# Optimization experiments

Measured on AMD Instinct MI355X. Metric: run time of the kernel, lower is better.

The kernel has to match this reference:

```python
import jax, jax.numpy as jnp
import numpy as np

CHAN = 24
INNER = 64
GROUPS = 8
M = 5
LAM = 1e-4
MAX_ITER = 25
BETA = 1.0
EPS = 1e-5
B, HH, WW = 128, 32, 32


def conv2d(x, w, b=None):
    # NCHW, OIHW, 3x3 SAME conv (padding = kernel//2)
    y = jax.lax.conv_general_dilated(x, w, (1, 1), 'SAME',
                                     dimension_numbers=('NCHW', 'OIHW', 'NCHW'))
    if b is not None:
        y = y + b[None, :, None, None]
    return y


def group_norm(x, g, b):
    bsz, c, h, w = x.shape
    xg = x.reshape(bsz, GROUPS, c // GROUPS, h, w)
    mu = xg.mean(axis=(2, 3, 4), keepdims=True)
    var = xg.var(axis=(2, 3, 4), keepdims=True)
    xn = ((xg - mu) / jnp.sqrt(var + EPS)).reshape(bsz, c, h, w)
    return xn * g[None, :, None, None] + b[None, :, None, None]


def batch_norm(x, g, b):
    # training-mode batch statistics over (N, H, W)
    mu = x.mean(axis=(0, 2, 3), keepdims=True)
    var = x.var(axis=(0, 2, 3), keepdims=True)
    return (x - mu) / jnp.sqrt(var + EPS) * g[None, :, None, None] + b[None, :, None, None]


def resnet_f(p, z, x):
    c1w, g1g, g1b, c2w, g2g, g2b, g3g, g3b = p
    y = group_norm(jax.nn.relu(conv2d(z, c1w)), g1g, g1b)
    return group_norm(jax.nn.relu(z + group_norm(x + conv2d(y, c2w), g2g, g2b)), g3g, g3b)


def anderson(f, x0):
    # Anderson acceleration, fixed MAX_ITER iterations (no host-sync tol break).
    bsz = x0.shape[0]
    d = x0.size // bsz
    X = jnp.zeros((bsz, M, d), x0.dtype)
    Fm = jnp.zeros((bsz, M, d), x0.dtype)
    f0 = f(x0).reshape(bsz, -1)
    X = X.at[:, 0].set(x0.reshape(bsz, -1))
    Fm = Fm.at[:, 0].set(f0)
    X = X.at[:, 1].set(f0)
    Fm = Fm.at[:, 1].set(f(f0.reshape(x0.shape)).reshape(bsz, -1))
    for k in range(2, MAX_ITER):
        n = min(k, M)
        G = Fm[:, :n] - X[:, :n]                       # [b, n, d]
        Hm = jnp.zeros((bsz, n + 1, n + 1), x0.dtype)
        Hm = Hm.at[:, 0, 1:].set(1.0).at[:, 1:, 0].set(1.0)
        Hm = Hm.at[:, 1:, 1:].set(jnp.einsum('bnd,bmd->bnm', G, G)
                                  + LAM * jnp.eye(n, dtype=x0.dtype)[None])
        yv = jnp.zeros((bsz, n + 1, 1), x0.dtype).at[:, 0, 0].set(1.0)
        alpha = jnp.linalg.solve(Hm, yv)[:, 1:, 0]     # [b, n]
        xnew = (BETA * jnp.einsum('bn,bnd->bd', alpha, Fm[:, :n])
                + (1.0 - BETA) * jnp.einsum('bn,bnd->bd', alpha, X[:, :n]))
        X = X.at[:, k % M].set(xnew)
        Fm = Fm.at[:, k % M].set(f(xnew.reshape(x0.shape)).reshape(bsz, -1))
    return X[:, (MAX_ITER - 1) % M].reshape(x0.shape)


def setup_inputs() -> dict:
    key = jax.random.key(0)
    ks = jax.random.split(key, 8)
    inp = {
        'x': jax.random.normal(ks[0], (B, 3, HH, WW), jnp.float32),
        'pre_conv_w': jax.random.normal(ks[1], (CHAN, 3, 3, 3), jnp.float32) * 0.1,
        'pre_conv_b': jnp.zeros((CHAN,), jnp.float32),
        'pre_bn_g': jnp.ones((CHAN,), jnp.float32),
        'pre_bn_b': jnp.zeros((CHAN,), jnp.float32),
        'f_conv1_w': jax.random.normal(ks[2], (INNER, CHAN, 3, 3), jnp.float32) * 0.01,
        'gn1_g': jnp.ones((INNER,), jnp.float32),
        'gn1_b': jnp.zeros((INNER,), jnp.float32),
        'f_conv2_w': jax.random.normal(ks[3], (CHAN, INNER, 3, 3), jnp.float32) * 0.01,
        'gn2_g': jnp.ones((CHAN,), jnp.float32),
        'gn2_b': jnp.zeros((CHAN,), jnp.float32),
        'gn3_g': jnp.ones((CHAN,), jnp.float32),
        'gn3_b': jnp.zeros((CHAN,), jnp.float32),
        'post_bn_g': jnp.ones((CHAN,), jnp.float32),
        'post_bn_b': jnp.zeros((CHAN,), jnp.float32),
        'fc_w': jax.random.normal(ks[4], (10, CHAN * 4 * 4), jnp.float32) * 0.05,
        'fc_b': jnp.zeros((10,), jnp.float32),
    }
    return inp


def reference(x, pre_conv_w, pre_conv_b, pre_bn_g, pre_bn_b,
              f_conv1_w, gn1_g, gn1_b, f_conv2_w, gn2_g, gn2_b, gn3_g, gn3_b,
              post_bn_g, post_bn_b, fc_w, fc_b):
    # pre: conv + BatchNorm
    xp = batch_norm(conv2d(x, pre_conv_w, pre_conv_b), pre_bn_g, pre_bn_b)
    p = (f_conv1_w, gn1_g, gn1_b, f_conv2_w, gn2_g, gn2_b, gn3_g, gn3_b)
    # DEQ fixed-point solve (eval path: train=False returns the fixed point)
    z_star = anderson(lambda z: resnet_f(p, z, xp), jnp.zeros_like(xp))
    z = resnet_f(p, z_star, xp)
    # post: relu -> BN -> avgpool(8,8) -> flatten -> linear
    h = batch_norm(jax.nn.relu(z), post_bn_g, post_bn_b)
    bsz, c, hh, ww = h.shape
    pooled = h.reshape(bsz, c, hh // 8, 8, ww // 8, 8).mean(axis=(3, 5))  # [B,C,4,4]
    return pooled.reshape(bsz, -1) @ fc_w.T + fc_b
```

## Files before the change

kernel.cpp:

```cpp
#include <hip/hip_runtime.h>
#include <hip/hip_bf16.h>

typedef __hip_bfloat16 bf16;
typedef unsigned short ushortT;
typedef __attribute__((ext_vector_type(8))) short short8;
typedef __attribute__((ext_vector_type(4))) float f32x4;

#define BB 128
#define CHAN 24
#define INNER 64
#define HW 1024
#define DD (CHAN*HW)

constexpr size_t cBD = (size_t)BB*DD;
constexpr size_t cYB = (size_t)BB*INNER*HW;

__device__ __attribute__((aligned(16))) ushortT g_xp[cBD];
__device__ __attribute__((aligned(16))) ushortT g_X[5*cBD];
__device__ __attribute__((aligned(16))) ushortT g_F[5*cBD];
__device__ __attribute__((aligned(16))) ushortT g_G[5*cBD];
__device__ __attribute__((aligned(16))) ushortT g_yb[cYB];
__device__ __attribute__((aligned(16))) ushortT g_tb[cBD];
__device__ __attribute__((aligned(16))) ushortT g_w1m[9*64*32];
__device__ __attribute__((aligned(16))) ushortT g_w2m[9*24*64];
__device__ __attribute__((aligned(16))) float g_stats2a[48];
__device__ __attribute__((aligned(16))) float g_stats2b[48];
__device__ __attribute__((aligned(16))) float g_gn1sum[BB*8*2];
__device__ __attribute__((aligned(16))) float g_gn2sum[BB*24*2];
__device__ __attribute__((aligned(16))) float g_gn3p[BB*4*16];
__device__ __attribute__((aligned(16))) float g_gramp[BB*4*5*5];
__device__ __attribute__((aligned(16))) float g_gram[BB*25];
__device__ __attribute__((aligned(16))) float g_pooled[BB*CHAN*16];
__device__ __attribute__((aligned(16))) float g_params[5120];
__device__ unsigned g_isbf16;

#define P_PCW 0
#define P_PCB 648
#define P_PBG 672
#define P_PBB 696
#define P_G1G 720
#define P_G1B 784
#define P_G2G 848
#define P_G2B 872
#define P_G3G 896
#define P_G3B 920
#define P_POG 944
#define P_POB 968
#define P_FCW 992
#define P_FCB 4832

__device__ __forceinline__ size_t aidx(int b, int icv, int pix){
  return (((size_t)b*3 + icv)*1024 + (size_t)pix)*8;
}
__device__ __forceinline__ float rdin(const void* p, int i){
  if (g_isbf16) return __bfloat162float(((const bf16*)p)[i]);
  return ((const float*)p)[i];
}
__device__ __forceinline__ float b2f(ushortT u){
  unsigned v = ((unsigned)u) << 16;
  return __builtin_bit_cast(float, v);
}
__device__ __forceinline__ ushortT f2b(float f){
  unsigned u = __builtin_bit_cast(unsigned, f);
  u += 0x7FFFu + ((u >> 16) & 1u);
  return (ushortT)(u >> 16);
}
__device__ __forceinline__ void ld24c(const ushortT* base, int b, int pix, float* o){
  #pragma unroll
  for (int icv=0;icv<3;icv++){
    short8 v = *(const short8*)&base[aidx(b,icv,pix)];
    #pragma unroll
    for (int j=0;j<8;j++) o[icv*8+j] = b2f((ushortT)v[j]);
  }
}
__device__ __forceinline__ void st24c(ushortT* base, int b, int pix, const float* i){
  #pragma unroll
  for (int icv=0;icv<3;icv++){
    short8 v;
    #pragma unroll
    for (int j=0;j<8;j++) v[j] = (short)f2b(i[icv*8+j]);
    *(short8*)&base[aidx(b,icv,pix)] = v;
  }
}

__global__ void detect_k(const void* g1g){
  if (threadIdx.x==0 && blockIdx.x==0){
    unsigned u = *(const unsigned*)g1g;
    g_isbf16 = (u == 0x3F803F80u) ? 1u : 0u;
  }
}

__global__ void cvt_params_k(const void* pcw, const void* pcb, const void* pbg, const void* pbb,
                             const void* g1g, const void* g1b, const void* g2g, const void* g2b,
                             const void* g3g, const void* g3b, const void* pog, const void* pob,
                             const void* fcw, const void* fcb){
  int t = threadIdx.x;
  for (int i=t;i<648;i+=256)  g_params[P_PCW+i]=rdin(pcw,i);
  for (int i=t;i<24;i+=256) { g_params[P_PCB+i]=rdin(pcb,i);
                              g_params[P_PBG+i]=rdin(pbg,i);
                              g_params[P_PBB+i]=rdin(pbb,i);
                              g_params[P_G2G+i]=rdin(g2g,i);
                              g_params[P_G2B+i]=rdin(g2b,i);
                              g_params[P_G3G+i]=rdin(g3g,i);
                              g_params[P_G3B+i]=rdin(g3b,i);
                              g_params[P_POG+i]=rdin(pog,i);
                              g_params[P_POB+i]=rdin(pob,i); }
  for (int i=t;i<64;i+=256) { g_params[P_G1G+i]=rdin(g1g,i);
                              g_params[P_G1B+i]=rdin(g1b,i); }
  for (int i=t;i<3840;i+=256) g_params[P_FCW+i]=rdin(fcw,i);
  for (int i=t;i<10;i+=256)   g_params[P_FCB+i]=rdin(fcb,i);
  for (int i=t;i<48;i+=256) { g_stats2a[i]=0.f; g_stats2b[i]=0.f; }
}

__global__ void wtm_k(const void* w1, const void* w2){
  int t = blockIdx.x*256 + threadIdx.x;
  if (t < 9*64*32){
    int ic = t & 31, oc = (t>>5)&63, s9 = t>>11;
    float v = (ic<24) ? rdin(w1, (oc*24+ic)*9 + s9) : 0.f;
    g_w1m[t] = f2b(v);
  }
  int u = t - 9*64*32;
  if (u >= 0 && u < 9*24*64){
    int ic = u & 63; int rest = u >> 6; int oc = rest % 24; int s9 = rest / 24;
    g_w2m[u] = f2b(rdin(w2, (oc*64+ic)*9 + s9));
  }
}

__global__ void zeroX0_k(){
  size_t i = ((size_t)blockIdx.x*256 + threadIdx.x)*8;
  short8 z = {0,0,0,0,0,0,0,0};
  *(short8*)&g_X[i] = z;
  if (blockIdx.x < 8) g_gn1sum[blockIdx.x*256 + threadIdx.x] = 0.f;
}
__global__ void copyF0toX1_k(){
  size_t i = ((size_t)blockIdx.x*256 + threadIdx.x)*8;
  *(short8*)&g_X[cBD + i] = *(const short8*)&g_F[i];
  if (blockIdx.x < 8) g_gn1sum[blockIdx.x*256 + threadIdx.x] = 0.f;
}

__global__ void preconv_k(const void* __restrict__ x){
  int id = blockIdx.x*256 + threadIdx.x;
  int b = id >> 10, pix = id & 1023;
  int yy = pix >> 5, xx = pix & 31;
  float acc[24];
  #pragma unroll
  for (int oc=0;oc<24;oc++) acc[oc] = g_params[P_PCB+oc];
  for (int ic=0; ic<3; ic++)
    for (int ky=0; ky<3; ky++){
      int gy = yy+ky-1; if (gy<0||gy>=32) continue;
      for (int kx=0;kx<3;kx++){
        int gx = xx+kx-1; if (gx<0||gx>=32) continue;
        float v = rdin(x, ((b*3+ic)*32+gy)*32+gx);
        #pragma unroll
        for (int oc=0;oc<24;oc++)
          acc[oc] += v * g_params[P_PCW+(oc*3+ic)*9+ky*3+kx];
      }
    }
  st24c(g_tb, b, pix, acc);
}

template<bool RELU>
__global__ void bnstat2_k(int which){
  const ushortT* src = (which==0) ? g_tb : (g_F + 4*cBD);
  float* dst = (which==0) ? g_stats2a : g_stats2b;
  __shared__ float sRed[48];
  int b = blockIdx.x >> 2, seg = blockIdx.x & 3;
  int t = threadIdx.x;
  if (t < 48) sRed[t] = 0.f;
  __syncthreads();
  int icv = t >> 6, pl = t & 63;
  float p0[8], p1[8];
  #pragma unroll
  for (int e=0;e<8;e++){ p0[e]=0.f; p1[e]=0.f; }
  for (int it=0; it<4; it++){
    int pix = seg*256 + it*64 + pl;
    short8 v = *(const short8*)&src[aidx(b,icv,pix)];
    #pragma unroll
    for (int e=0;e<8;e++){
      float f = b2f((ushortT)v[e]); if (RELU) f = fmaxf(f,0.f);
      p0[e]+=f; p1[e]+=f*f;
    }
  }
  #pragma unroll
  for (int e=0;e<8;e++){
    atomicAdd(&sRed[(icv*8+e)*2],   p0[e]);
    atomicAdd(&sRed[(icv*8+e)*2+1], p1[e]);
  }
  __syncthreads();
  if (t < 48) atomicAdd(&dst[t], sRed[t]);
}

__global__ void bn_apply_k(){
  int id = blockIdx.x*256+threadIdx.x;
  int b = id >> 10, pix = id & 1023;
  const float inv = 1.f/(BB*HW);
  float tv[24], ov[24];
  ld24c(g_tb, b, pix, tv);
  #pragma unroll
  for (int c=0;c<24;c++){
    float mean = g_stats2a[c*2]*inv;
    float var = fmaxf(g_stats2a[c*2+1]*inv - mean*mean, 0.f);
    float rstd = rsqrtf(var + 1e-5f);
    ov[c] = (tv[c]-mean)*rstd*g_params[P_PBG+c] + g_params[P_PBB+c];
  }
  st24c(g_xp, b, pix, ov);
}

__launch_bounds__(256, 2)
__global__ void conv1_k(int s){
  __shared__ ushortT sMem[29312];
  ushortT* sA = sMem;
  ushortT* sW = sMem + 10880;
  const int tid = threadIdx.x;
  const int lane = tid & 63, wv = tid >> 6;
  const int mLane = lane & 15, q = lane >> 4;
  const int b = blockIdx.x >> 2, yt = blockIdx.x & 3;
  const ushortT* __restrict__ Xs = g_X + (size_t)s*cBD;
  if (blockIdx.x < 24) g_gn2sum[blockIdx.x*256 + tid] = 0.f;
  for (int i = tid; i < 1360; i += 256){
    int icv = i & 3, apix = i >> 2;
    int yl = apix / 34, xl = apix - yl*34;
    int gy = yt*8 - 1 + yl, gx = xl - 1;
    short8 v = {0,0,0,0,0,0,0,0};
    if (gy >= 0 && gy < 32 && gx >= 0 && gx < 32 && icv < 3)
      v = *(const short8*)&Xs[aidx(b, icv, gy*32 + gx)];
    *(short8*)&sA[(size_t)(apix*4 + (icv ^ (apix&3)))*8] = v;
  }
  for (int i = tid; i < 2304; i += 256){
    int icv = i & 3, rest = i >> 2;
    int oc = rest & 63, s9 = rest >> 6;
    short8 v = *(const short8*)&g_w1m[(size_t)((s9*64 + oc)*32) + icv*8];
    *(short8*)&sW[(size_t)((s9*64+oc)*4 + (icv ^ (oc&3)))*8] = v;
  }
  __syncthreads();
  f32x4 acc[4][4];
  #pragma unroll
  for (int mt=0;mt<4;mt++)
    #pragma unroll
    for (int nt=0;nt<4;nt++) acc[mt][nt] = (f32x4){0.f,0.f,0.f,0.f};
  for (int s9=0; s9<9; s9++){
    int ky = s9/3, kx = s9 - ky*3;
    short8 bfr[4];
    #pragma unroll
    for (int nt=0;nt<4;nt++){
      int oc = nt*16 + mLane;
      bfr[nt] = *(const short8*)&sW[(size_t)((s9*64+oc)*4 + (q ^ (oc&3)))*8];
    }
    #pragma unroll
    for (int mt=0;mt<4;mt++){
      int g = wv*4+mt;
      int apix = ((g>>1) + ky)*34 + (g&1)*16 + mLane + kx;
      short8 afr = *(const short8*)&sA[(size_t)(apix*4 + (q ^ (apix&3)))*8];
      #pragma unroll
      for (int nt=0;nt<4;nt++)
        acc[mt][nt] = __builtin_amdgcn_mfma_f32_16x16x32_bf16(afr, bfr[nt], acc[mt][nt], 0,0,0);
    }
  }
  __syncthreads();
  ushortT* sOut = sMem;
  #pragma unroll
  for (int mt=0;mt<4;mt++){
    int g = wv*4+mt;
    #pragma unroll
    for (int nt=0;nt<4;nt++){
      int oc = nt*16 + mLane;
      #pragma unroll
      for (int r=0;r<4;r++){
        int pix = (g>>1)*32 + (g&1)*16 + q*4 + r;
        sOut[pix*64 + oc] = f2b(fmaxf(acc[mt][nt][r], 0.f));
      }
    }
  }
  __syncthreads();
  float s0=0.f, s1=0.f;
  size_t gbase = ((size_t)b*1024 + yt*256)*64;
  for (int c = tid; c < 2048; c += 256){
    short8 v = *(const short8*)&sOut[c*8];
    *(short8*)&g_yb[gbase + (size_t)c*8] = v;
    #pragma unroll
    for (int j=0;j<8;j++){ float f = b2f((ushortT)v[j]); s0 += f; s1 += f*f; }
  }
  s0 += __shfl_down(s0,32); s1 += __shfl_down(s1,32);
  s0 += __shfl_down(s0,16); s1 += __shfl_down(s1,16);
  s0 += __shfl_down(s0, 8); s1 += __shfl_down(s1, 8);
  if (lane < 8){
    atomicAdd(&g_gn1sum[(b*8+lane)*2],   s0);
    atomicAdd(&g_gn1sum[(b*8+lane)*2+1], s1);
  }
}

__launch_bounds__(256, 2)
__global__ void conv2_k(){
  __shared__ ushortT sMem[35584];
  __shared__ float sAff[128];
  ushortT* sA = sMem;
  ushortT* sW = sMem + 21760;
  const int tid = threadIdx.x;
  const int lane = tid & 63, wv = tid >> 6;
  const int mLane = lane & 15, q = lane >> 4;
  const int b = blockIdx.x >> 2, yt = blockIdx.x & 3;
  if (tid < 64){
    int c = tid, gr = c>>3;
    float S = g_gn1sum[(b*8+gr)*2], Q = g_gn1sum[(b*8+gr)*2+1];
    float mean = S*(1.f/8192.f);
    float var = fmaxf(Q*(1.f/8192.f) - mean*mean, 0.f);
    float rstd = rsqrtf(var + 1e-5f);
    float sc = rstd*g_params[P_G1G+c];
    sAff[c] = sc; sAff[64+c] = g_params[P_G1B+c] - mean*sc;
  }
  __syncthreads();
  for (int i = tid; i < 2720; i += 256){
    int icv = i & 7, apix = i >> 3;
    int yl = apix / 34, xl = apix - yl*34;
    int gy = yt*8 - 1 + yl, gx = xl - 1;
    short8 v = {0,0,0,0,0,0,0,0};
    if (gy >= 0 && gy < 32 && gx >= 0 && gx < 32){
      short8 raw = *(const short8*)&g_yb[((size_t)b*1024 + gy*32+gx)*64 + icv*8];
      #pragma unroll
      for (int j=0;j<8;j++){
        int c = icv*8+j;
        v[j] = (short)f2b(b2f((ushortT)raw[j])*sAff[c] + sAff[64+c]);
      }
    }
    *(short8*)&sA[(size_t)(apix*8 + (icv ^ (apix&7)))*8] = v;
  }
  for (int i = tid; i < 1728; i += 256){
    int icv = i & 7, rest = i >> 3;
    int oc = rest % 24, s9 = rest / 24;
    short8 v = *(const short8*)&g_w2m[(size_t)((s9*24+oc)*64) + icv*8];
    *(short8*)&sW[(size_t)((s9*24+oc)*8 + (icv ^ (oc&7)))*8] = v;
  }
  __syncthreads();
  f32x4 acc[4][2];
  #pragma unroll
  for (int mt=0;mt<4;mt++){ acc[mt][0]=(f32x4){0.f,0.f,0.f,0.f}; acc[mt][1]=(f32x4){0.f,0.f,0.f,0.f}; }
  const bool nt1ok = (mLane < 8);
  for (int s9=0; s9<9; s9++){
    int ky = s9/3, kx = s9 - ky*3;
    #pragma unroll
    for (int ks=0; ks<2; ks++){
      int ib = ks*4;
      short8 bfr[2];
      { int oc = mLane;
        bfr[0] = *(const short8*)&sW[(size_t)((s9*24+oc)*8 + ((ib+q) ^ (oc&7)))*8]; }
      if (nt1ok){
        int oc = 16 + mLane;
        bfr[1] = *(const short8*)&sW[(size_t)((s9*24+oc)*8 + ((ib+q) ^ (oc&7)))*8];
      } else bfr[1] = (short8){0,0,0,0,0,0,0,0};
      #pragma unroll
      for (int mt=0;mt<4;mt++){
        int g = wv*4+mt;
        int apix = ((g>>1) + ky)*34 + (g&1)*16 + mLane + kx;
        short8 afr = *(const short8*)&sA[(size_t)(apix*8 + ((ib+q) ^ (apix&7)))*8];
        acc[mt][0] = __builtin_amdgcn_mfma_f32_16x16x32_bf16(afr, bfr[0], acc[mt][0], 0,0,0);
        acc[mt][1] = __builtin_amdgcn_mfma_f32_16x16x32_bf16(afr, bfr[1], acc[mt][1], 0,0,0);
      }
    }
  }
  #pragma unroll
  for (int nt=0;nt<2;nt++){
    int oc = nt*16 + mLane;
    bool ok = (oc < 24);
    int icv = oc >> 3, e = oc & 7;
    float s0=0.f, s1=0.f;
    if (ok){
      #pragma unroll
      for (int mt=0;mt<4;mt++){
        int g = wv*4+mt;
        #pragma unroll
        for (int r=0;r<4;r++){
          int pix = (yt*8 + (g>>1))*32 + (g&1)*16 + q*4 + r;
          size_t o = aidx(b, icv, pix) + e;
          float v = acc[mt][nt][r] + b2f(g_xp[o]);
          g_tb[o] = f2b(v);
          s0 += v; s1 += v*v;
        }
      }
    }
    s0 += __shfl_down(s0,32); s1 += __shfl_down(s1,32);
    s0 += __shfl_down(s0,16); s1 += __shfl_down(s1,16);
    if (lane < 16 && ok){
      atomicAdd(&g_gn2sum[(b*24+oc)*2],   s0);
      atomicAdd(&g_gn2sum[(b*24+oc)*2+1], s1);
    }
  }
}

__launch_bounds__(256)
__global__ void fuse_a_k(int s){
  __shared__ float sM2[8], sR2[8], sSc2[24], sSb2[24];
  __shared__ float sRed[64];
  const int b = blockIdx.x>>2, seg = blockIdx.x&3;
  const int t = threadIdx.x;
  if (t < 8){
    float S = g_gn2sum[(b*24+t*3)*2]   + g_gn2sum[(b*24+t*3+1)*2]   + g_gn2sum[(b*24+t*3+2)*2];
    float Q = g_gn2sum[(b*24+t*3)*2+1] + g_gn2sum[(b*24+t*3+1)*2+1] + g_gn2sum[(b*24+t*3+2)*2+1];
    float m = S*(1.f/3072.f);
    sM2[t] = m;
    sR2[t] = rsqrtf(fmaxf(Q*(1.f/3072.f) - m*m, 0.f) + 1e-5f);
  }
  __syncthreads();
  if (t < 24){
    int g = t/3;
    float sc = sR2[g]*g_params[P_G2G+t];
    sSc2[t] = sc; sSb2[t] = g_params[P_G2B+t] - sM2[g]*sc;
  }
  __syncthreads();
  const int pix = seg*256 + t;
  float tv[24], xv[24];
  ld24c(g_tb, b, pix, tv);
  ld24c(g_X + (size_t)s*cBD, b, pix, xv);
  float p0[8], p1[8];
  #pragma unroll
  for (int g=0;g<8;g++){ p0[g]=0.f; p1[g]=0.f; }
  #pragma unroll
  for (int c=0;c<24;c++){
    int g = c/3;
    float v = fmaxf(xv[c] + tv[c]*sSc2[c] + sSb2[c], 0.f);
    p0[g] += v; p1[g] += v*v;
  }
  #pragma unroll
  for (int g=0;g<8;g++){
    for (int off=32;off>0;off>>=1){ p0[g]+=__shfl_down(p0[g],off,64); p1[g]+=__shfl_down(p1[g],off,64); }
  }
  int lane = t&63, wv = t>>6;
  if (lane==0){
    #pragma unroll
    for (int g=0;g<8;g++){ sRed[wv*16+g*2]=p0[g]; sRed[wv*16+g*2+1]=p1[g]; }
  }
  __syncthreads();
  if (t < 16){
    g_gn3p[(b*4+seg)*16 + t] = sRed[t]+sRed[16+t]+sRed[32+t]+sRed[48+t];
  }
}

__launch_bounds__(256)
__global__ void fuse_b_k(int s, int nv){
  __shared__ float sM2[8], sR2[8], sM3[8], sR3[8];
  __shared__ float sSc2[24], sSb2[24], sSc3[24], sSb3[24];
  __shared__ float sRedG[4][5];
  const int b = blockIdx.x>>2, seg = blockIdx.x&3;
  const int t = threadIdx.x;
  if (t < 8){
    float S = g_gn2sum[(b*24+t*3)*2]   + g_gn2sum[(b*24+t*3+1)*2]   + g_gn2sum[(b*24+t*3+2)*2];
    float Q = g_gn2sum[(b*24+t*3)*2+1] + g_gn2sum[(b*24+t*3+1)*2+1] + g_gn2sum[(b*24+t*3+2)*2+1];
    float m = S*(1.f/3072.f);
    sM2[t] = m;
    sR2[t] = rsqrtf(fmaxf(Q*(1.f/3072.f) - m*m, 0.f) + 1e-5f);
    float S3 = g_gn3p[(b*4+0)*16+t*2]   + g_gn3p[(b*4+1)*16+t*2]
             + g_gn3p[(b*4+2)*16+t*2]   + g_gn3p[(b*4+3)*16+t*2];
    float Q3 = g_gn3p[(b*4+0)*16+t*2+1] + g_gn3p[(b*4+1)*16+t*2+1]
             + g_gn3p[(b*4+2)*16+t*2+1] + g_gn3p[(b*4+3)*16+t*2+1];
    float m3 = S3*(1.f/3072.f);
    sM3[t] = m3;
    sR3[t] = rsqrtf(fmaxf(Q3*(1.f/3072.f) - m3*m3, 0.f) + 1e-5f);
  }
  __syncthreads();
  if (t < 24){
    int g = t/3;
    float sc2 = sR2[g]*g_params[P_G2G+t];
    sSc2[t] = sc2; sSb2[t] = g_params[P_G2B+t] - sM2[g]*sc2;
    float sc3 = sR3[g]*g_params[P_G3G+t];
    sSc3[t] = sc3; sSb3[t] = g_params[P_G3B+t] - sM3[g]*sc3;
  }
  __syncthreads();
  const int pix = seg*256 + t;
  float tv[24], xv[24], fv[24], gl[24];
  ld24c(g_tb, b, pix, tv);
  ld24c(g_X + (size_t)s*cBD, b, pix, xv);
  #pragma unroll
  for (int c=0;c<24;c++){
    float v = fmaxf(xv[c] + tv[c]*sSc2[c] + sSb2[c], 0.f);
    fv[c] = v*sSc3[c] + sSb3[c];
    float g = fv[c] - xv[c];
    gl[c] = b2f(f2b(g));
  }
  st24c(g_F + (size_t)s*cBD, b, pix, fv);
  st24c(g_G + (size_t)s*cBD, b, pix, gl);
  if (nv == 0) return;
  float part[5];
  #pragma unroll
  for (int j=0;j<5;j++) part[j]=0.f;
  #pragma unroll
  for (int j=0;j<5;j++){
    if (j>=nv) continue;
    float acc=0.f;
    if (j==s){
      #pragma unroll
      for (int c=0;c<24;c++) acc += gl[c]*gl[c];
    } else {
      float gv[24];
      ld24c(g_G + (size_t)j*cBD, b, pix, gv);
      #pragma unroll
      for (int c=0;c<24;c++) acc += gl[c]*gv[c];
    }
    part[j]=acc;
  }
  int lane = t&63, wv = t>>6;
  #pragma unroll
  for (int j=0;j<5;j++){
    float v = part[j];
    for (int off=32;off>0;off>>=1) v += __shfl_down(v,off,64);
    if (lane==0 && j<nv) sRedG[wv][j] = v;
  }
  __syncthreads();
  if (t < 5 && t < nv){
    float v = sRedG[0][t]+sRedG[1][t]+sRedG[2][t]+sRedG[3][t];
    g_gramp[((b*4+seg)*5 + s)*5 + t] = v;
  }
}

template<int N>
__device__ __forceinline__ void chol_alpha(const float Kf[5][5], float* alpha){
  double K[N][N];
  #pragma unroll
  for (int i=0;i<N;i++)
    #pragma unroll
    for (int j=0;j<N;j++)
      K[i][j] = (double)Kf[i][j] + (i==j ? 1e-4 : 0.0);
  #pragma unroll
  for (int c=0;c<N;c++){
    double d = K[c][c];
    #pragma unroll
    for (int k2=0;k2<c;k2++) d -= K[c][k2]*K[c][k2];
    d = sqrt(fmax(d, 1e-300));
    K[c][c] = d;
    double inv = 1.0/d;
    #pragma unroll
    for (int r=c+1;r<N;r++){
      double v = K[r][c];
      #pragma unroll
      for (int k2=0;k2<c;k2++) v -= K[r][k2]*K[c][k2];
      K[r][c] = v*inv;
    }
  }
  double y[N];
  #pragma unroll
  for (int i=0;i<N;i++){
    double v = 1.0;
    #pragma unroll
    for (int j=0;j<i;j++) v -= K[i][j]*y[j];
    y[i] = v / K[i][i];
  }
  double w[N];
  #pragma unroll
  for (int i=N-1;i>=0;i--){
    double v = y[i];
    #pragma unroll
    for (int j=i+1;j<N;j++) v -= K[j][i]*w[j];
    w[i] = v / K[i][i];
  }
  double sum = 0.0;
  #pragma unroll
  for (int i=0;i<N;i++) sum += w[i];
  double invs = 1.0/sum;
  #pragma unroll
  for (int i=0;i<N;i++) alpha[i] = (float)(w[i]*invs);
}

__global__ void xns_k(int s, int n, int rA, int nvA, int rB, int nvB){
  __shared__ float sAlpha[5];
  if (blockIdx.x < 8) g_gn1sum[blockIdx.x*256 + threadIdx.x] = 0.f;
  const int b = blockIdx.x >> 2, ch = blockIdx.x & 3;
  const int t = threadIdx.x;
  if (t == 0){
    float Kf[5][5];
    for (int i=0;i<n;i++)
      for (int j=0;j<n;j++) Kf[i][j] = g_gram[b*25 + i*5 + j];
    for (int j=0;j<nvA;j++){
      float v = g_gramp[((b*4+0)*5 + rA)*5 + j] + g_gramp[((b*4+1)*5 + rA)*5 + j]
              + g_gramp[((b*4+2)*5 + rA)*5 + j] + g_gramp[((b*4+3)*5 + rA)*5 + j];
      Kf[rA][j] = v; Kf[j][rA] = v;
    }
    if (rB >= 0){
      for (int j=0;j<nvB;j++){
        float v = g_gramp[((b*4+0)*5 + rB)*5 + j] + g_gramp[((b*4+1)*5 + rB)*5 + j]
                + g_gramp[((b*4+2)*5 + rB)*5 + j] + g_gramp[((b*4+3)*5 + rB)*5 + j];
        Kf[rB][j] = v; Kf[j][rB] = v;
      }
    }
    if (ch == 0){
      for (int j=0;j<nvA;j++){ g_gram[b*25+rA*5+j]=Kf[rA][j]; g_gram[b*25+j*5+rA]=Kf[rA][j]; }
      if (rB >= 0)
        for (int j=0;j<nvB;j++){ g_gram[b*25+rB*5+j]=Kf[rB][j]; g_gram[b*25+j*5+rB]=Kf[rB][j]; }
    }
    float al[5];
    if (n==2) chol_alpha<2>(Kf, al);
    else if (n==3) chol_alpha<3>(Kf, al);
    else if (n==4) chol_alpha<4>(Kf, al);
    else chol_alpha<5>(Kf, al);
    for (int j=0;j<n;j++) sAlpha[j] = al[j];
  }
  __syncthreads();
  float a[5];
  for (int j=0;j<n;j++) a[j] = sAlpha[j];
  const size_t base = (size_t)b*DD + (size_t)ch*6144;
  #pragma unroll
  for (int i=0;i<3;i++){
    size_t off = base + (size_t)i*2048 + (size_t)t*8;
    float acc[8];
    #pragma unroll
    for (int e=0;e<8;e++) acc[e]=0.f;
    for (int j=0;j<n;j++){
      short8 f = *(const short8*)&g_F[(size_t)j*cBD + off];
      float aj = a[j];
      #pragma unroll
      for (int e=0;e<8;e++) acc[e] += aj*b2f((ushortT)f[e]);
    }
    short8 o;
    #pragma unroll
    for (int e=0;e<8;e++) o[e] = (short)f2b(acc[e]);
    *(short8*)&g_X[(size_t)s*cBD + off] = o;
  }
}

__global__ void post_pool_k(){
  int i = blockIdx.x*256+threadIdx.x; if (i >= BB*CHAN*16) return;
  const ushortT* z = g_F + 4*cBD;
  int pw = i&3, ph=(i>>2)&3, c=(i>>4)%CHAN, bi=i/(CHAN*16);
  int icv = c>>3, e = c&7;
  float inv = 1.f/(BB*HW);
  float mean = g_stats2b[c*2]*inv;
  float var = fmaxf(g_stats2b[c*2+1]*inv - mean*mean, 0.f);
  float rstd = rsqrtf(var + 1e-5f);
  float gg=g_params[P_POG+c], bv=g_params[P_POB+c];
  float s=0.f;
  for (int dy=0;dy<8;dy++)
    for (int dx=0;dx<8;dx++){
      int pix = (ph*8+dy)*32 + pw*8+dx;
      float v = fmaxf(b2f(z[aidx(bi,icv,pix) + e]), 0.f);
      s += (v-mean)*rstd*gg + bv;
    }
  g_pooled[i] = s*(1.f/64.f);
}

__global__ void fc_k(void* __restrict__ out){
  int i = blockIdx.x*256+threadIdx.x; if (i>=BB*10) return;
  int j=i%10, bi=i/10;
  float s = g_params[P_FCB+j];
  for (int k=0;k<384;k++) s += g_pooled[bi*384+k]*g_params[P_FCW+j*384+k];
  if (g_isbf16) ((bf16*)out)[i] = __float2bfloat16(s);
  else ((float*)out)[i] = s;
}

extern "C" void kernel_launch(void* const* d_in, const int* in_sizes, int n_in,
                              void* d_out, int out_size, void* d_ws, size_t ws_size,
                              hipStream_t stream){
  const void* x   = d_in[0];
  const void* pcw = d_in[1];
  const void* pcb = d_in[2];
  const void* pbg = d_in[3];
  const void* pbb = d_in[4];
  const void* w1  = d_in[5];
  const void* g1g = d_in[6];
  const void* g1b = d_in[7];
  const void* w2  = d_in[8];
  const void* g2g = d_in[9];
  const void* g2b = d_in[10];
  const void* g3g = d_in[11];
  const void* g3b = d_in[12];
  const void* pog = d_in[13];
  const void* pob = d_in[14];
  const void* fcw = d_in[15];
  const void* fcb = d_in[16];
  (void)d_ws; (void)ws_size;

  const int gPix = (int)(BB*HW/256);

  auto feval = [&](int s, int nv){
    conv1_k<<<512,256,0,stream>>>(s);
    conv2_k<<<512,256,0,stream>>>();
    fuse_a_k<<<512,256,0,stream>>>(s);
    fuse_b_k<<<512,256,0,stream>>>(s, nv);
  };

  detect_k<<<1,64,0,stream>>>(g1g);
  cvt_params_k<<<1,256,0,stream>>>(pcw,pcb,pbg,pbb,g1g,g1b,g2g,g2b,g3g,g3b,pog,pob,fcw,fcb);
  wtm_k<<<126,256,0,stream>>>(w1, w2);

  preconv_k<<<gPix,256,0,stream>>>(x);
  bnstat2_k<false><<<512,192,0,stream>>>(0);
  bn_apply_k<<<gPix,256,0,stream>>>();

  zeroX0_k<<<1536,256,0,stream>>>();
  feval(0, 1);
  copyF0toX1_k<<<1536,256,0,stream>>>();
  feval(1, 2);

  for (int k=2;k<25;k++){
    int n = k<5 ? k : 5;
    int s = k%5;
    int nv = (k+1<5)?(k+1):5;
    if (k==2) xns_k<<<512,256,0,stream>>>(s, 2, 0, 1, 1, 2);
    else      xns_k<<<512,256,0,stream>>>(s, n, (k-1)%5, n, -1, 0);
    feval(s, (k<24) ? nv : 0);
  }

  bnstat2_k<true><<<512,192,0,stream>>>(1);
  post_pool_k<<<(BB*CHAN*16+255)/256,256,0,stream>>>();
  fc_k<<<(BB*10+255)/256,256,0,stream>>>(d_out);
}
```

Measured before the change: 1.577 ms.

## Fuse GroupNorm, Gram, Anderson solve and mixing into one per-sample kernel

Merges fuse_a, fuse_b and xns into a single 1024-thread-per-sample kernel. It computes GN2/GN3 stats in-block, writes F and G, builds the Gram row, solves for alpha in one thread and forms the next X directly. It also folds the BN stats into preconv, skips conv1 on the zero first iterate via zeroed yb, and merges the post-pool and FC kernels. Launches and global round-trips drop, at the cost of only 128 blocks for the fused step and a serial Cholesky inside the block.

```diff
diff --git a/kernel.cpp b/kernel.cpp
--- a/kernel.cpp
+++ b/kernel.cpp
@@ -27,10 +27,7 @@
 __device__ __attribute__((aligned(16))) float g_stats2b[48];
 __device__ __attribute__((aligned(16))) float g_gn1sum[BB*8*2];
 __device__ __attribute__((aligned(16))) float g_gn2sum[BB*24*2];
-__device__ __attribute__((aligned(16))) float g_gn3p[BB*4*16];
-__device__ __attribute__((aligned(16))) float g_gramp[BB*4*5*5];
 __device__ __attribute__((aligned(16))) float g_gram[BB*25];
-__device__ __attribute__((aligned(16))) float g_pooled[BB*CHAN*16];
 __device__ __attribute__((aligned(16))) float g_params[5120];
 __device__ unsigned g_isbf16;
 
@@ -126,19 +123,18 @@
   }
 }
 
-__global__ void zeroX0_k(){
-  size_t i = ((size_t)blockIdx.x*256 + threadIdx.x)*8;
+__global__ void zero0_k(){
+  size_t base = ((size_t)blockIdx.x*256 + threadIdx.x)*8;
   short8 z = {0,0,0,0,0,0,0,0};
-  *(short8*)&g_X[i] = z;
-  if (blockIdx.x < 8) g_gn1sum[blockIdx.x*256 + threadIdx.x] = 0.f;
-}
-__global__ void copyF0toX1_k(){
-  size_t i = ((size_t)blockIdx.x*256 + threadIdx.x)*8;
-  *(short8*)&g_X[cBD + i] = *(const short8*)&g_F[i];
-  if (blockIdx.x < 8) g_gn1sum[blockIdx.x*256 + threadIdx.x] = 0.f;
+  *(short8*)&g_yb[base] = z;
+  if (blockIdx.x < 1536) *(short8*)&g_X[base] = z;
+  int t = blockIdx.x*256 + threadIdx.x;
+  if (blockIdx.x < 8)  g_gn1sum[t] = 0.f;
+  if (blockIdx.x < 24) g_gn2sum[t] = 0.f;
 }
 
 __global__ void preconv_k(const void* __restrict__ x){
+  __shared__ float sR2d[4*48];
   int id = blockIdx.x*256 + threadIdx.x;
   int b = id >> 10, pix = id & 1023;
   int yy = pix >> 5, xx = pix & 31;
@@ -157,37 +153,18 @@
       }
     }
   st24c(g_tb, b, pix, acc);
-}
-
-template<bool RELU>
-__global__ void bnstat2_k(int which){
-  const ushortT* src = (which==0) ? g_tb : (g_F + 4*cBD);
-  float* dst = (which==0) ? g_stats2a : g_stats2b;
-  __shared__ float sRed[48];
-  int b = blockIdx.x >> 2, seg = blockIdx.x & 3;
-  int t = threadIdx.x;
-  if (t < 48) sRed[t] = 0.f;
-  __syncthreads();
-  int icv = t >> 6, pl = t & 63;
-  float p0[8], p1[8];
-  #pragma unroll
-  for (int e=0;e<8;e++){ p0[e]=0.f; p1[e]=0.f; }
-  for (int it=0; it<4; it++){
-    int pix = seg*256 + it*64 + pl;
-    short8 v = *(const short8*)&src[aidx(b,icv,pix)];
-    #pragma unroll
-    for (int e=0;e<8;e++){
-      float f = b2f((ushortT)v[e]); if (RELU) f = fmaxf(f,0.f);
-      p0[e]+=f; p1[e]+=f*f;
-    }
-  }
-  #pragma unroll
-  for (int e=0;e<8;e++){
-    atomicAdd(&sRed[(icv*8+e)*2],   p0[e]);
-    atomicAdd(&sRed[(icv*8+e)*2+1], p1[e]);
-  }
-  __syncthreads();
-  if (t < 48) atomicAdd(&dst[t], sRed[t]);
+  int lane = threadIdx.x & 63, wv = threadIdx.x >> 6;
+  #pragma unroll
+  for (int c=0;c<24;c++){
+    float r = acc[c], q = acc[c]*acc[c];
+    #pragma unroll
+    for (int off=32;off;off>>=1){ r += __shfl_down(r,off,64); q += __shfl_down(q,off,64); }
+    if (lane==0){ sR2d[wv*48+c*2]=r; sR2d[wv*48+c*2+1]=q; }
+  }
+  __syncthreads();
+  if (threadIdx.x < 48)
+    atomicAdd(&g_stats2a[threadIdx.x],
+      sR2d[threadIdx.x] + sR2d[48+threadIdx.x] + sR2d[96+threadIdx.x] + sR2d[144+threadIdx.x]);
 }
 
 __global__ void bn_apply_k(){
@@ -386,12 +363,66 @@
   }
 }
 
-__launch_bounds__(256)
-__global__ void fuse_a_k(int s){
-  __shared__ float sM2[8], sR2[8], sSc2[24], sSb2[24];
-  __shared__ float sRed[64];
-  const int b = blockIdx.x>>2, seg = blockIdx.x&3;
+template<int N>
+__device__ __forceinline__ void chol_alpha(const float Kf[5][5], float* alpha){
+  double K[N][N];
+  #pragma unroll
+  for (int i=0;i<N;i++)
+    #pragma unroll
+    for (int j=0;j<N;j++)
+      K[i][j] = (double)Kf[i][j] + (i==j ? 1e-4 : 0.0);
+  #pragma unroll
+  for (int c=0;c<N;c++){
+    double d = K[c][c];
+    #pragma unroll
+    for (int k2=0;k2<c;k2++) d -= K[c][k2]*K[c][k2];
+    d = sqrt(fmax(d, 1e-300));
+    K[c][c] = d;
+    double inv = 1.0/d;
+    #pragma unroll
+    for (int r=c+1;r<N;r++){
+      double v = K[r][c];
+      #pragma unroll
+      for (int k2=0;k2<c;k2++) v -= K[r][k2]*K[c][k2];
+      K[r][c] = v*inv;
+    }
+  }
+  double y[N];
+  #pragma unroll
+  for (int i=0;i<N;i++){
+    double v = 1.0;
+    #pragma unroll
+    for (int j=0;j<i;j++) v -= K[i][j]*y[j];
+    y[i] = v / K[i][i];
+  }
+  double w[N];
+  #pragma unroll
+  for (int i=N-1;i>=0;i--){
+    double v = y[i];
+    #pragma unroll
+    for (int j=i+1;j<N;j++) v -= K[j][i]*w[j];
+    w[i] = v / K[i][i];
+  }
+  double sum = 0.0;
+  #pragma unroll
+  for (int i=0;i<N;i++) sum += w[i];
+  double invs = 1.0/sum;
+  #pragma unroll
+  for (int i=0;i<N;i++) alpha[i] = (float)(w[i]*invs);
+}
+
+__launch_bounds__(1024)
+__global__ void fuse_k(int s, int n, int snext){
+  __shared__ float sM2[8], sR2[8], sM3[8], sR3[8];
+  __shared__ float sSc2[24], sSb2[24], sSc3[24], sSb3[24];
+  __shared__ float sRed[16*16];
+  __shared__ float sRedG[16*5];
+  __shared__ float sAlpha[5];
+  __shared__ float sStat[16*48];
+  const int b = blockIdx.x;
   const int t = threadIdx.x;
+  const int lane = t & 63, wv = t >> 6;
+  if (t < 16) g_gn1sum[b*16 + t] = 0.f;
   if (t < 8){
     float S = g_gn2sum[(b*24+t*3)*2]   + g_gn2sum[(b*24+t*3+1)*2]   + g_gn2sum[(b*24+t*3+2)*2];
     float Q = g_gn2sum[(b*24+t*3)*2+1] + g_gn2sum[(b*24+t*3+1)*2+1] + g_gn2sum[(b*24+t*3+2)*2+1];
@@ -406,241 +437,169 @@
     sSc2[t] = sc; sSb2[t] = g_params[P_G2B+t] - sM2[g]*sc;
   }
   __syncthreads();
-  const int pix = seg*256 + t;
-  float tv[24], xv[24];
-  ld24c(g_tb, b, pix, tv);
-  ld24c(g_X + (size_t)s*cBD, b, pix, xv);
+  float xv[24], v[24];
+  ld24c(g_tb, b, t, v);
+  ld24c(g_X + (size_t)s*cBD, b, t, xv);
   float p0[8], p1[8];
   #pragma unroll
   for (int g=0;g<8;g++){ p0[g]=0.f; p1[g]=0.f; }
   #pragma unroll
   for (int c=0;c<24;c++){
+    float val = fmaxf(xv[c] + v[c]*sSc2[c] + sSb2[c], 0.f);
+    v[c] = val;
     int g = c/3;
-    float v = fmaxf(xv[c] + tv[c]*sSc2[c] + sSb2[c], 0.f);
-    p0[g] += v; p1[g] += v*v;
+    p0[g] += val; p1[g] += val*val;
   }
   #pragma unroll
   for (int g=0;g<8;g++){
-    for (int off=32;off>0;off>>=1){ p0[g]+=__shfl_down(p0[g],off,64); p1[g]+=__shfl_down(p1[g],off,64); }
-  }
-  int lane = t&63, wv = t>>6;
+    #pragma unroll
+    for (int off=32;off;off>>=1){ p0[g]+=__shfl_down(p0[g],off,64); p1[g]+=__shfl_down(p1[g],off,64); }
+  }
   if (lane==0){
     #pragma unroll
     for (int g=0;g<8;g++){ sRed[wv*16+g*2]=p0[g]; sRed[wv*16+g*2+1]=p1[g]; }
   }
   __syncthreads();
-  if (t < 16){
-    g_gn3p[(b*4+seg)*16 + t] = sRed[t]+sRed[16+t]+sRed[32+t]+sRed[48+t];
-  }
-}
-
-__launch_bounds__(256)
-__global__ void fuse_b_k(int s, int nv){
-  __shared__ float sM2[8], sR2[8], sM3[8], sR3[8];
-  __shared__ float sSc2[24], sSb2[24], sSc3[24], sSb3[24];
-  __shared__ float sRedG[4][5];
-  const int b = blockIdx.x>>2, seg = blockIdx.x&3;
-  const int t = threadIdx.x;
   if (t < 8){
-    float S = g_gn2sum[(b*24+t*3)*2]   + g_gn2sum[(b*24+t*3+1)*2]   + g_gn2sum[(b*24+t*3+2)*2];
-    float Q = g_gn2sum[(b*24+t*3)*2+1] + g_gn2sum[(b*24+t*3+1)*2+1] + g_gn2sum[(b*24+t*3+2)*2+1];
+    float S=0.f, Q=0.f;
+    #pragma unroll
+    for (int w=0;w<16;w++){ S += sRed[w*16+t*2]; Q += sRed[w*16+t*2+1]; }
     float m = S*(1.f/3072.f);
-    sM2[t] = m;
-    sR2[t] = rsqrtf(fmaxf(Q*(1.f/3072.f) - m*m, 0.f) + 1e-5f);
-    float S3 = g_gn3p[(b*4+0)*16+t*2]   + g_gn3p[(b*4+1)*16+t*2]
-             + g_gn3p[(b*4+2)*16+t*2]   + g_gn3p[(b*4+3)*16+t*2];
-    float Q3 = g_gn3p[(b*4+0)*16+t*2+1] + g_gn3p[(b*4+1)*16+t*2+1]
-             + g_gn3p[(b*4+2)*16+t*2+1] + g_gn3p[(b*4+3)*16+t*2+1];
-    float m3 = S3*(1.f/3072.f);
-    sM3[t] = m3;
-    sR3[t] = rsqrtf(fmaxf(Q3*(1.f/3072.f) - m3*m3, 0.f) + 1e-5f);
+    sM3[t] = m;
+    sR3[t] = rsqrtf(fmaxf(Q*(1.f/3072.f) - m*m, 0.f) + 1e-5f);
   }
   __syncthreads();
   if (t < 24){
     int g = t/3;
-    float sc2 = sR2[g]*g_params[P_G2G+t];
-    sSc2[t] = sc2; sSb2[t] = g_params[P_G2B+t] - sM2[g]*sc2;
-    float sc3 = sR3[g]*g_params[P_G3G+t];
-    sSc3[t] = sc3; sSb3[t] = g_params[P_G3B+t] - sM3[g]*sc3;
-  }
-  __syncthreads();
-  const int pix = seg*256 + t;
-  float tv[24], xv[24], fv[24], gl[24];
-  ld24c(g_tb, b, pix, tv);
-  ld24c(g_X + (size_t)s*cBD, b, pix, xv);
-  #pragma unroll
-  for (int c=0;c<24;c++){
-    float v = fmaxf(xv[c] + tv[c]*sSc2[c] + sSb2[c], 0.f);
-    fv[c] = v*sSc3[c] + sSb3[c];
-    float g = fv[c] - xv[c];
-    gl[c] = b2f(f2b(g));
-  }
-  st24c(g_F + (size_t)s*cBD, b, pix, fv);
-  st24c(g_G + (size_t)s*cBD, b, pix, gl);
-  if (nv == 0) return;
-  float part[5];
-  #pragma unroll
-  for (int j=0;j<5;j++) part[j]=0.f;
-  #pragma unroll
-  for (int j=0;j<5;j++){
-    if (j>=nv) continue;
-    float acc=0.f;
-    if (j==s){
-      #pragma unroll
-      for (int c=0;c<24;c++) acc += gl[c]*gl[c];
-    } else {
-      float gv[24];
-      ld24c(g_G + (size_t)j*cBD, b, pix, gv);
-      #pragma unroll
-      for (int c=0;c<24;c++) acc += gl[c]*gv[c];
-    }
-    part[j]=acc;
-  }
-  int lane = t&63, wv = t>>6;
-  #pragma unroll
-  for (int j=0;j<5;j++){
-    float v = part[j];
-    for (int off=32;off>0;off>>=1) v += __shfl_down(v,off,64);
-    if (lane==0 && j<nv) sRedG[wv][j] = v;
-  }
-  __syncthreads();
-  if (t < 5 && t < nv){
-    float v = sRedG[0][t]+sRedG[1][t]+sRedG[2][t]+sRedG[3][t];
-    g_gramp[((b*4+seg)*5 + s)*5 + t] = v;
-  }
-}
-
-template<int N>
-__device__ __forceinline__ void chol_alpha(const float Kf[5][5], float* alpha){
-  double K[N][N];
-  #pragma unroll
-  for (int i=0;i<N;i++)
-    #pragma unroll
-    for (int j=0;j<N;j++)
-      K[i][j] = (double)Kf[i][j] + (i==j ? 1e-4 : 0.0);
-  #pragma unroll
-  for (int c=0;c<N;c++){
-    double d = K[c][c];
-    #pragma unroll
-    for (int k2=0;k2<c;k2++) d -= K[c][k2]*K[c][k2];
-    d = sqrt(fmax(d, 1e-300));
-    K[c][c] = d;
-    double inv = 1.0/d;
-    #pragma unroll
-    for (int r=c+1;r<N;r++){
-      double v = K[r][c];
-      #pragma unroll
-      for (int k2=0;k2<c;k2++) v -= K[r][k2]*K[c][k2];
-      K[r][c] = v*inv;
-    }
-  }
-  double y[N];
-  #pragma unroll
-  for (int i=0;i<N;i++){
-    double v = 1.0;
-    #pragma unroll
-    for (int j=0;j<i;j++) v -= K[i][j]*y[j];
-    y[i] = v / K[i][i];
-  }
-  double w[N];
-  #pragma unroll
-  for (int i=N-1;i>=0;i--){
-    double v = y[i];
-    #pragma unroll
-    for (int j=i+1;j<N;j++) v -= K[j][i]*w[j];
-    w[i] = v / K[i][i];
-  }
-  double sum = 0.0;
-  #pragma unroll
-  for (int i=0;i<N;i++) sum += w[i];
-  double invs = 1.0/sum;
-  #pragma unroll
-  for (int i=0;i<N;i++) alpha[i] = (float)(w[i]*invs);
-}
-
-__global__ void xns_k(int s, int n, int rA, int nvA, int rB, int nvB){
-  __shared__ float sAlpha[5];
-  if (blockIdx.x < 8) g_gn1sum[blockIdx.x*256 + threadIdx.x] = 0.f;
-  const int b = blockIdx.x >> 2, ch = blockIdx.x & 3;
-  const int t = threadIdx.x;
-  if (t == 0){
-    float Kf[5][5];
-    for (int i=0;i<n;i++)
-      for (int j=0;j<n;j++) Kf[i][j] = g_gram[b*25 + i*5 + j];
-    for (int j=0;j<nvA;j++){
-      float v = g_gramp[((b*4+0)*5 + rA)*5 + j] + g_gramp[((b*4+1)*5 + rA)*5 + j]
-              + g_gramp[((b*4+2)*5 + rA)*5 + j] + g_gramp[((b*4+3)*5 + rA)*5 + j];
-      Kf[rA][j] = v; Kf[j][rA] = v;
-    }
-    if (rB >= 0){
-      for (int j=0;j<nvB;j++){
-        float v = g_gramp[((b*4+0)*5 + rB)*5 + j] + g_gramp[((b*4+1)*5 + rB)*5 + j]
-                + g_gramp[((b*4+2)*5 + rB)*5 + j] + g_gramp[((b*4+3)*5 + rB)*5 + j];
-        Kf[rB][j] = v; Kf[j][rB] = v;
-      }
-    }
-    if (ch == 0){
-      for (int j=0;j<nvA;j++){ g_gram[b*25+rA*5+j]=Kf[rA][j]; g_gram[b*25+j*5+rA]=Kf[rA][j]; }
-      if (rB >= 0)
-        for (int j=0;j<nvB;j++){ g_gram[b*25+rB*5+j]=Kf[rB][j]; g_gram[b*25+j*5+rB]=Kf[rB][j]; }
-    }
-    float al[5];
-    if (n==2) chol_alpha<2>(Kf, al);
-    else if (n==3) chol_alpha<3>(Kf, al);
-    else if (n==4) chol_alpha<4>(Kf, al);
-    else chol_alpha<5>(Kf, al);
-    for (int j=0;j<n;j++) sAlpha[j] = al[j];
-  }
-  __syncthreads();
-  float a[5];
-  for (int j=0;j<n;j++) a[j] = sAlpha[j];
-  const size_t base = (size_t)b*DD + (size_t)ch*6144;
-  #pragma unroll
-  for (int i=0;i<3;i++){
-    size_t off = base + (size_t)i*2048 + (size_t)t*8;
-    float acc[8];
-    #pragma unroll
-    for (int e=0;e<8;e++) acc[e]=0.f;
-    for (int j=0;j<n;j++){
-      short8 f = *(const short8*)&g_F[(size_t)j*cBD + off];
-      float aj = a[j];
-      #pragma unroll
-      for (int e=0;e<8;e++) acc[e] += aj*b2f((ushortT)f[e]);
-    }
-    short8 o;
-    #pragma unroll
-    for (int e=0;e<8;e++) o[e] = (short)f2b(acc[e]);
-    *(short8*)&g_X[(size_t)s*cBD + off] = o;
-  }
-}
-
-__global__ void post_pool_k(){
-  int i = blockIdx.x*256+threadIdx.x; if (i >= BB*CHAN*16) return;
+    float sc = sR3[g]*g_params[P_G3G+t];
+    sSc3[t] = sc; sSb3[t] = g_params[P_G3B+t] - sM3[g]*sc;
+  }
+  __syncthreads();
+  float fv[24];
+  #pragma unroll
+  for (int c=0;c<24;c++) fv[c] = v[c]*sSc3[c] + sSb3[c];
+  st24c(g_F + (size_t)s*cBD, b, t, fv);
+
+  if (n > 0){
+    float gl[24];
+    #pragma unroll
+    for (int c=0;c<24;c++) gl[c] = b2f(f2b(fv[c] - xv[c]));
+    st24c(g_G + (size_t)s*cBD, b, t, gl);
+    float part[5];
+    #pragma unroll
+    for (int j=0;j<5;j++) part[j] = 0.f;
+    #pragma unroll
+    for (int j=0;j<5;j++){
+      if (j >= n) continue;
+      float acc = 0.f;
+      if (j == s){
+        #pragma unroll
+        for (int c=0;c<24;c++) acc += gl[c]*gl[c];
+      } else {
+        float gv[24];
+        ld24c(g_G + (size_t)j*cBD, b, t, gv);
+        #pragma unroll
+        for (int c=0;c<24;c++) acc += gl[c]*gv[c];
+      }
+      part[j] = acc;
+    }
+    #pragma unroll
+    for (int j=0;j<5;j++){
+      float vv = part[j];
+      #pragma unroll
+      for (int off=32;off;off>>=1) vv += __shfl_down(vv,off,64);
+      if (lane==0) sRedG[wv*5+j] = vv;
+    }
+    __syncthreads();
+    if (t == 0){
+      for (int j=0;j<n;j++){
+        float vv = 0.f;
+        for (int w=0;w<16;w++) vv += sRedG[w*5+j];
+        g_gram[b*25+s*5+j] = vv;
+        g_gram[b*25+j*5+s] = vv;
+      }
+      float Kf[5][5];
+      for (int i=0;i<n;i++)
+        for (int j=0;j<n;j++) Kf[i][j] = g_gram[b*25+i*5+j];
+      float al[5];
+      if (n==1) al[0]=1.f;
+      else if (n==2) chol_alpha<2>(Kf, al);
+      else if (n==3) chol_alpha<3>(Kf, al);
+      else if (n==4) chol_alpha<4>(Kf, al);
+      else chol_alpha<5>(Kf, al);
+      for (int j=0;j<n;j++) sAlpha[j] = al[j];
+    }
+    __syncthreads();
+    float acc[24];
+    #pragma unroll
+    for (int c=0;c<24;c++) acc[c] = 0.f;
+    #pragma unroll
+    for (int j=0;j<5;j++){
+      if (j >= n) continue;
+      float aj = sAlpha[j];
+      if (j == s){
+        #pragma unroll
+        for (int c=0;c<24;c++) acc[c] += aj*b2f(f2b(fv[c]));
+      } else {
+        float tv2[24];
+        ld24c(g_F + (size_t)j*cBD, b, t, tv2);
+        #pragma unroll
+        for (int c=0;c<24;c++) acc[c] += aj*tv2[c];
+      }
+    }
+    st24c(g_X + (size_t)snext*cBD, b, t, acc);
+  } else {
+    #pragma unroll
+    for (int c=0;c<24;c++){
+      float r = fmaxf(b2f(f2b(fv[c])), 0.f);
+      float q = r*r;
+      #pragma unroll
+      for (int off=32;off;off>>=1){ r += __shfl_down(r,off,64); q += __shfl_down(q,off,64); }
+      if (lane==0){ sStat[wv*48+c*2]=r; sStat[wv*48+c*2+1]=q; }
+    }
+    __syncthreads();
+    if (t < 48){
+      float vv = 0.f;
+      #pragma unroll
+      for (int w=0;w<16;w++) vv += sStat[w*48+t];
+      atomicAdd(&g_stats2b[t], vv);
+    }
+  }
+}
+
+__global__ void postfc_k(void* __restrict__ out){
+  __shared__ float sPool[384];
+  __shared__ float sMean[24], sRstd[24];
+  int b = blockIdx.x, t = threadIdx.x;
+  if (t < 24){
+    const float inv = 1.f/(BB*HW);
+    float mean = g_stats2b[t*2]*inv;
+    float var = fmaxf(g_stats2b[t*2+1]*inv - mean*mean, 0.f);
+    sMean[t] = mean; sRstd[t] = rsqrtf(var + 1e-5f);
+  }
+  __syncthreads();
   const ushortT* z = g_F + 4*cBD;
-  int pw = i&3, ph=(i>>2)&3, c=(i>>4)%CHAN, bi=i/(CHAN*16);
-  int icv = c>>3, e = c&7;
-  float inv = 1.f/(BB*HW);
-  float mean = g_stats2b[c*2]*inv;
-  float var = fmaxf(g_stats2b[c*2+1]*inv - mean*mean, 0.f);
-  float rstd = rsqrtf(var + 1e-5f);
-  float gg=g_params[P_POG+c], bv=g_params[P_POB+c];
-  float s=0.f;
-  for (int dy=0;dy<8;dy++)
-    for (int dx=0;dx<8;dx++){
-      int pix = (ph*8+dy)*32 + pw*8+dx;
-      float v = fmaxf(b2f(z[aidx(bi,icv,pix) + e]), 0.f);
-      s += (v-mean)*rstd*gg + bv;
-    }
-  g_pooled[i] = s*(1.f/64.f);
-}
-
-__global__ void fc_k(void* __restrict__ out){
-  int i = blockIdx.x*256+threadIdx.x; if (i>=BB*10) return;
-  int j=i%10, bi=i/10;
-  float s = g_params[P_FCB+j];
-  for (int k=0;k<384;k++) s += g_pooled[bi*384+k]*g_params[P_FCW+j*384+k];
-  if (g_isbf16) ((bf16*)out)[i] = __float2bfloat16(s);
-  else ((float*)out)[i] = s;
+  for (int i=t; i<384; i+=256){
+    int c = i>>4, bin = i&15, ph = bin>>2, pw = bin&3;
+    int icv = c>>3, e = c&7;
+    float gg = g_params[P_POG+c], bv = g_params[P_POB+c];
+    float mean = sMean[c], rstd = sRstd[c];
+    float sum = 0.f;
+    for (int dy=0;dy<8;dy++)
+      for (int dx=0;dx<8;dx++){
+        int pix = (ph*8+dy)*32 + pw*8+dx;
+        float vv = fmaxf(b2f(z[aidx(b,icv,pix) + e]), 0.f);
+        sum += (vv-mean)*rstd*gg + bv;
+      }
+    sPool[i] = sum*(1.f/64.f);
+  }
+  __syncthreads();
+  if (t < 10){
+    float s2 = g_params[P_FCB+t];
+    for (int k2=0;k2<384;k2++) s2 += sPool[k2]*g_params[P_FCW+t*384+k2];
+    if (g_isbf16) ((bf16*)out)[b*10+t] = __float2bfloat16(s2);
+    else ((float*)out)[b*10+t] = s2;
+  }
 }
 
 extern "C" void kernel_launch(void* const* d_in, const int* in_sizes, int n_in,
@@ -663,40 +622,30 @@
   const void* pob = d_in[14];
   const void* fcw = d_in[15];
   const void* fcb = d_in[16];
-  (void)d_ws; (void)ws_size;
-
-  const int gPix = (int)(BB*HW/256);
-
-  auto feval = [&](int s, int nv){
-    conv1_k<<<512,256,0,stream>>>(s);
-    conv2_k<<<512,256,0,stream>>>();
-    fuse_a_k<<<512,256,0,stream>>>(s);
-    fuse_b_k<<<512,256,0,stream>>>(s, nv);
-  };
+  (void)d_ws; (void)ws_size; (void)in_sizes; (void)n_in; (void)out_size;
 
   detect_k<<<1,64,0,stream>>>(g1g);
   cvt_params_k<<<1,256,0,stream>>>(pcw,pcb,pbg,pbb,g1g,g1b,g2g,g2b,g3g,g3b,pog,pob,fcw,fcb);
   wtm_k<<<126,256,0,stream>>>(w1, w2);
 
-  preconv_k<<<gPix,256,0,stream>>>(x);
-  bnstat2_k<false><<<512,192,0,stream>>>(0);
-  bn_apply_k<<<gPix,256,0,stream>>>();
-
-  zeroX0_k<<<1536,256,0,stream>>>();
-  feval(0, 1);
-  copyF0toX1_k<<<1536,256,0,stream>>>();
-  feval(1, 2);
-
-  for (int k=2;k<25;k++){
-    int n = k<5 ? k : 5;
+  preconv_k<<<512,256,0,stream>>>(x);
+  bn_apply_k<<<512,256,0,stream>>>();
+
+  zero0_k<<<4096,256,0,stream>>>();
+  conv2_k<<<512,256,0,stream>>>();
+  fuse_k<<<128,1024,0,stream>>>(0, 1, 1);
+
+  for (int k=1;k<25;k++){
     int s = k%5;
-    int nv = (k+1<5)?(k+1):5;
-    if (k==2) xns_k<<<512,256,0,stream>>>(s, 2, 0, 1, 1, 2);
-    else      xns_k<<<512,256,0,stream>>>(s, n, (k-1)%5, n, -1, 0);
-    feval(s, (k<24) ? nv : 0);
-  }
-
-  bnstat2_k<true><<<512,192,0,stream>>>(1);
-  post_pool_k<<<(BB*CHAN*16+255)/256,256,0,stream>>>();
-  fc_k<<<(BB*10+255)/256,256,0,stream>>>(d_out);
-}
+    conv1_k<<<512,256,0,stream>>>(s);
+    conv2_k<<<512,256,0,stream>>>();
+    if (k < 24){
+      int n = (k+1 < 5) ? (k+1) : 5;
+      fuse_k<<<128,1024,0,stream>>>(s, n, (k+1)%5);
+    } else {
+      fuse_k<<<128,1024,0,stream>>>(s, 0, -1);
+    }
+  }
+
+  postfc_k<<<128,256,0,stream>>>(d_out);
+}
```

Result: faster. 1.452 ms (-7.9%).
